# Kernel tuning notes

Hardware: AMD Instinct MI355X
Metric: run time of the kernel (lower is better)

The kernel has to match this reference:

```python
import jax, jax.numpy as jnp
import numpy as np

N_NODES = 32768
AGENTS = 32            # agents per sample (fully connected)
N_SAMPLES = N_NODES // AGENTS
N_EDGES = N_SAMPLES * AGENTS * (AGENTS - 1)  # 1,015,808
D = 64                 # latent_size
EDGE_DIM = 2
Z_DIM = 2 * D + EDGE_DIM  # CGConv concat width = 130
BN_EPS = 1e-5


def _build_block_edge_index():
    # fully-connected (no self-loop) blocks of AGENTS nodes, offset per sample
    a = np.arange(AGENTS)
    src, dst = np.meshgrid(a, a, indexing='ij')
    mask = src != dst
    src, dst = src[mask], dst[mask]              # [AGENTS*(AGENTS-1)]
    offs = (np.arange(N_SAMPLES) * AGENTS)[:, None]
    src = (src[None, :] + offs).reshape(-1)
    dst = (dst[None, :] + offs).reshape(-1)
    return jnp.asarray(np.stack([src, dst]), dtype=jnp.int64)


def setup_inputs() -> dict:
    key = jax.random.key(0)
    ks = jax.random.split(key, 16)
    x = jax.random.normal(ks[0], (N_NODES, D), dtype=jnp.float32)
    edge_index = _build_block_edge_index()                      # [2, E]
    edge_attr = jax.random.normal(ks[1], (N_EDGES, EDGE_DIM), dtype=jnp.float32)
    s = 1.0 / np.sqrt(Z_DIM)
    params = {}
    for li, base in ((1, 2), (2, 8)):
        params[f'Wf{li}'] = jax.random.uniform(ks[base + 0], (Z_DIM, D), jnp.float32, -s, s)
        params[f'bf{li}'] = jax.random.uniform(ks[base + 1], (D,), jnp.float32, -s, s)
        params[f'Ws{li}'] = jax.random.uniform(ks[base + 2], (Z_DIM, D), jnp.float32, -s, s)
        params[f'bs{li}'] = jax.random.uniform(ks[base + 3], (D,), jnp.float32, -s, s)
        params[f'gamma{li}'] = jnp.ones((D,), jnp.float32)
        params[f'beta{li}'] = jnp.zeros((D,), jnp.float32)
    return {'x': x, 'edge_index': edge_index, 'edge_attr': edge_attr, **params}


def _cgconv(x, edge_index, edge_attr, Wf, bf, Ws, bs, gamma, beta):
    src, dst = edge_index[0], edge_index[1]
    # z_ij = [x_i, x_j, e_ij], i = target (dst), j = source (src)
    z = jnp.concatenate([x[dst], x[src], edge_attr], axis=-1)       # [E, Z_DIM]
    m = jax.nn.sigmoid(z @ Wf + bf) * jax.nn.softplus(z @ Ws + bs)  # gated message
    agg = jax.ops.segment_sum(m, dst, num_segments=x.shape[0])      # scatter-add
    mu = jnp.mean(agg, axis=0)
    var = jnp.var(agg, axis=0)
    agg = (agg - mu) * jax.lax.rsqrt(var + BN_EPS) * gamma + beta   # train-mode BN
    return agg + x                                                  # residual


def reference(x, edge_index, edge_attr,
              Wf1, bf1, Ws1, bs1, gamma1, beta1,
              Wf2, bf2, Ws2, bs2, gamma2, beta2):
    h = jax.nn.relu(_cgconv(x, edge_index, edge_attr, Wf1, bf1, Ws1, bs1, gamma1, beta1))
    out = jax.nn.relu(_cgconv(h, edge_index, edge_attr, Wf2, bf2, Ws2, bs2, gamma2, beta2))
    return out
```

## Files before the change

### kernel.cpp

```cpp
#include <hip/hip_runtime.h>


#define NSAMP 1024
#define AG 32
#define DD 64
#define EPB 992
#define NN 32768
#define R1S 132

typedef float f4 __attribute__((ext_vector_type(4)));
typedef float f2 __attribute__((ext_vector_type(2)));

#define L2E 1.44269504088896340736f
#define BN_EPS_SCALED (1e-5 * (double)L2E * (double)L2E)

__device__ __forceinline__ void gacc(f4& acc, const f4 mf, const f4 ms) {
#pragma unroll
  for (int k = 0; k < 4; ++k) {
    float den = 1.0f + __builtin_amdgcn_exp2f(-mf[k]);
    float sig = __builtin_amdgcn_rcpf(den);
    float sp  = fmaxf(ms[k], 0.0f)
              + __builtin_amdgcn_logf(1.0f + __builtin_amdgcn_exp2f(-fabsf(ms[k])));
    acc[k] += sig * sp;
  }
}

template <int SRC>
__device__ __forceinline__ void gpass(const float* __restrict__ Wf,
                                      const float* __restrict__ bfv,
                                      const float* __restrict__ Ws,
                                      const float* __restrict__ bsv,
                                      const float* xb, float* R1, int t) {
  const int tx = t & 31, ty = t >> 5;
  const int q = tx >> 4;
  const int cc0 = (tx & 15) * 4;
  const float* wbase = (q ? Ws : Wf) + SRC * (64 * 64) + cc0;
  f4 acc[4];
  if constexpr (SRC == 0) {
    const float* bv = q ? bsv : bfv;
    f4 b = *(const f4*)(bv + cc0) * L2E;
#pragma unroll
    for (int r = 0; r < 4; ++r) acc[r] = b;
  } else {
    f4 z4 = {0.f, 0.f, 0.f, 0.f};
#pragma unroll
    for (int r = 0; r < 4; ++r) acc[r] = z4;
  }
#pragma unroll
  for (int k4 = 0; k4 < 16; ++k4) {
    const float* wp = wbase + k4 * 4 * 64;
    f4 w0 = *(const f4*)(wp);
    f4 w1 = *(const f4*)(wp + 64);
    f4 w2 = *(const f4*)(wp + 128);
    f4 w3 = *(const f4*)(wp + 192);
#pragma unroll
    for (int r = 0; r < 4; ++r) {
      f4 xv = *(const f4*)&xb[(ty * 4 + r) * 64 + k4 * 4];
      acc[r] += xv.x * w0 + xv.y * w1 + xv.z * w2 + xv.w * w3;
    }
  }
#pragma unroll
  for (int r = 0; r < 4; ++r)
    *(f4*)&R1[(ty * 4 + r) * R1S + q * 64 + cc0] = acc[r];
}

__device__ __forceinline__ void run_layer(
    int t, int s, const float* __restrict__ ea,
    const float* __restrict__ Wf, const float* __restrict__ bfv,
    const float* __restrict__ Ws, const float* __restrict__ bsv,
    float* xb, float* R1, double* __restrict__ stats,
    float* __restrict__ agg)
{
  const int i = t >> 3, c0 = (t & 7) * 8;

  gpass<0>(Wf, bfv, Ws, bsv, xb, R1, t);
  __syncthreads();
  const float* ri = &R1[i * R1S];
  f4 afa = *(const f4*)(ri + c0);
  f4 afb = *(const f4*)(ri + c0 + 4);
  f4 asa = *(const f4*)(ri + 64 + c0);
  f4 asb = *(const f4*)(ri + 64 + c0 + 4);
  __syncthreads();
  gpass<1>(Wf, bfv, Ws, bsv, xb, R1, t);

  f4 wf0a = *(const f4*)(Wf + 128 * 64 + c0);
  f4 wf0b = *(const f4*)(Wf + 128 * 64 + c0 + 4);
  f4 wf1a = *(const f4*)(Wf + 129 * 64 + c0);
  f4 wf1b = *(const f4*)(Wf + 129 * 64 + c0 + 4);
  f4 ws0a = *(const f4*)(Ws + 128 * 64 + c0);
  f4 ws0b = *(const f4*)(Ws + 128 * 64 + c0 + 4);
  f4 ws1a = *(const f4*)(Ws + 129 * 64 + c0);
  f4 ws1b = *(const f4*)(Ws + 129 * 64 + c0 + 4);
  __syncthreads();

  {
    const f2* esrc = ((const f2*)ea) + s * EPB;
    f2* ed = (f2*)xb;
    for (int u = t; u < EPB; u += 256) ed[u] = esrc[u] * L2E;
  }
  __syncthreads();

  f4 acc0 = {0.f, 0.f, 0.f, 0.f}, acc1 = {0.f, 0.f, 0.f, 0.f};
  for (int jj = 0; jj < 31; ++jj) {
    const int ge = (jj >= i) ? 1 : 0;
    const int j  = jj + ge;
    const int e  = j * 31 + i - 1 + ge;
    f2 eav = *(const f2*)&xb[e * 2];
    const float* gj = &R1[j * R1S];
    f4 bfa = *(const f4*)(gj + c0);
    f4 bfb = *(const f4*)(gj + c0 + 4);
    f4 bsa = *(const f4*)(gj + 64 + c0);
    f4 bsb = *(const f4*)(gj + 64 + c0 + 4);
    f4 mfa = afa + bfa + eav.x * wf0a + eav.y * wf1a;
    f4 mfb = afb + bfb + eav.x * wf0b + eav.y * wf1b;
    f4 msa = asa + bsa + eav.x * ws0a + eav.y * ws1a;
    f4 msb = asb + bsb + eav.x * ws0b + eav.y * ws1b;
    gacc(acc0, mfa, msa);
    gacc(acc1, mfb, msb);
  }

  float* ap = agg + (s * AG + i) * DD + c0;
  *(f4*)ap       = acc0;
  *(f4*)(ap + 4) = acc1;

  __syncthreads();
  if (t < 128) R1[t] = 0.f;
  __syncthreads();
#pragma unroll
  for (int k = 0; k < 4; ++k) {
    atomicAdd(&R1[c0 + k],          acc0[k]);
    atomicAdd(&R1[64 + c0 + k],     acc0[k] * acc0[k]);
    atomicAdd(&R1[c0 + 4 + k],      acc1[k]);
    atomicAdd(&R1[64 + c0 + 4 + k], acc1[k] * acc1[k]);
  }
  __syncthreads();
  if (t < 128) atomicAdd(&stats[t], (double)R1[t]);
}

__global__ __launch_bounds__(256, 4) void k_edge1(
    const float* __restrict__ x, const float* __restrict__ ea,
    const float* __restrict__ Wf, const float* __restrict__ bfv,
    const float* __restrict__ Ws, const float* __restrict__ bsv,
    float* __restrict__ agg, double* __restrict__ stats)
{
  __shared__ __align__(16) float xb[2048];
  __shared__ __align__(16) float R1[32 * R1S];
  const int t = threadIdx.x, s = blockIdx.x;
  {
    const f4* src = (const f4*)(x + s * AG * DD);
    f4* dst = (f4*)xb;
    dst[t]       = src[t] * L2E;
    dst[t + 256] = src[t + 256] * L2E;
  }
  __syncthreads();
  run_layer(t, s, ea, Wf, bfv, Ws, bsv, xb, R1, stats, agg);
}

__global__ __launch_bounds__(256, 4) void k_edge2(
    const float* __restrict__ x, const float* __restrict__ ea,
    const float* __restrict__ Wf, const float* __restrict__ bfv,
    const float* __restrict__ Ws, const float* __restrict__ bsv,
    const double* __restrict__ stats1, const float* __restrict__ gmv,
    const float* __restrict__ btv, float* __restrict__ hout,
    float* __restrict__ agg, double* __restrict__ stats2)
{
  __shared__ __align__(16) float xb[2048];
  __shared__ __align__(16) float R1[32 * R1S];
  const int t = threadIdx.x, s = blockIdx.x;
  const int i = t >> 3, c0 = (t & 7) * 8;

  if (t < 64) {
    double mu  = stats1[t] * (1.0 / NN);
    double var = stats1[64 + t] * (1.0 / NN) - mu * mu;
    float rs = (float)(1.0 / sqrt(var + BN_EPS_SCALED));
    float g  = gmv[t] * rs;
    R1[t]      = g;
    R1[64 + t] = btv[t] - (float)mu * g;
  }
  __syncthreads();
  {
    f4 sca = *(const f4*)&R1[c0],      scb = *(const f4*)&R1[c0 + 4];
    f4 sha = *(const f4*)&R1[64 + c0], shb = *(const f4*)&R1[64 + c0 + 4];
    const float* ap = agg + (s * AG + i) * DD + c0;
    f4 a0 = *(const f4*)ap, a1 = *(const f4*)(ap + 4);
    const f4* xg = (const f4*)(x + (s * AG + i) * DD + c0);
    f4 h0 = a0 * sca + sha + xg[0];
    f4 h1 = a1 * scb + shb + xg[1];
#pragma unroll
    for (int k = 0; k < 4; ++k) { h0[k] = fmaxf(h0[k], 0.f); h1[k] = fmaxf(h1[k], 0.f); }
    f4* hg = (f4*)(hout + (s * AG + i) * DD + c0);
    hg[0] = h0; hg[1] = h1;
    *(f4*)&xb[i * DD + c0]     = h0 * L2E;
    *(f4*)&xb[i * DD + c0 + 4] = h1 * L2E;
  }
  __syncthreads();
  run_layer(t, s, ea, Wf, bfv, Ws, bsv, xb, R1, stats2, agg);
}

__global__ __launch_bounds__(256) void k_norm(
    const float* __restrict__ agg, const double* __restrict__ stats,
    const float* __restrict__ gmv, const float* __restrict__ btv,
    float* __restrict__ outp)
{
  __shared__ __align__(16) float sc[DD];
  __shared__ __align__(16) float sh[DD];
  const int t = threadIdx.x;
  if (t < DD) {
    double mu  = stats[t] * (1.0 / NN);
    double var = stats[DD + t] * (1.0 / NN) - mu * mu;
    float rs = (float)(1.0 / sqrt(var + BN_EPS_SCALED));
    float g  = gmv[t] * rs;
    sc[t] = g;
    sh[t] = btv[t] - (float)mu * g;
  }
  __syncthreads();
  const int idx = blockIdx.x * 256 + t;
  const int c   = (idx * 4) & (DD - 1);
  f4 a = ((const f4*)agg)[idx];
  f4 h = ((const f4*)outp)[idx];
  f4 r = a * (*(const f4*)&sc[c]) + (*(const f4*)&sh[c]) + h;
#pragma unroll
  for (int k = 0; k < 4; ++k) r[k] = fmaxf(r[k], 0.0f);
  ((f4*)outp)[idx] = r;
}

extern "C" void kernel_launch(void* const* d_in, const int* in_sizes, int n_in,
                              void* d_out, int out_size, void* d_ws, size_t ws_size,
                              hipStream_t stream) {
  const float* x   = (const float*)d_in[0];
  const float* ea  = (const float*)d_in[2];
  const float* Wf1 = (const float*)d_in[3];
  const float* bf1 = (const float*)d_in[4];
  const float* Ws1 = (const float*)d_in[5];
  const float* bs1 = (const float*)d_in[6];
  const float* gm1 = (const float*)d_in[7];
  const float* bt1 = (const float*)d_in[8];
  const float* Wf2 = (const float*)d_in[9];
  const float* bf2 = (const float*)d_in[10];
  const float* Ws2 = (const float*)d_in[11];
  const float* bs2 = (const float*)d_in[12];
  const float* gm2 = (const float*)d_in[13];
  const float* bt2 = (const float*)d_in[14];

  double* stats = (double*)d_ws;
  float*  agg   = (float*)((char*)d_ws + 4096);
  float*  outp  = (float*)d_out;

  hipMemsetAsync(d_ws, 0, 2048, stream);
  k_edge1<<<NSAMP, 256, 0, stream>>>(x, ea, Wf1, bf1, Ws1, bs1, agg, stats);
  k_edge2<<<NSAMP, 256, 0, stream>>>(x, ea, Wf2, bf2, Ws2, bs2,
                                     stats, gm1, bt1, outp, agg, stats + 128);
  k_norm<<<NN * DD / 4 / 256, 256, 0, stream>>>(agg, stats + 128, gm2, bt2, outp);
}
```

Baseline: 247.2 us.

## Split each sample across two blocks and read inputs directly from global memory

Each sample is now handled by two blocks, each covering 16 target nodes, with 4 channels per thread instead of 8. The kernels raise launch bounds to 8 blocks per CU and drop the LDS staging buffers for x and the edge attributes, reading both straight from global or cache. The L2E scaling moves to after the projection, shuffles pre-reduce the BN statistics before the shared atomics, and separate agg buffers keep layer-1 reads apart from layer-2 writes. The aim is more parallelism and occupancy. The cost is that both blocks recompute the full 32-row source projection and the layer-2 input h, and more workspace is needed.

New measurement: 434.2 us. 75.6% more time.

```diff
diff --git a/kernel.cpp b/kernel.cpp
--- a/kernel.cpp
+++ b/kernel.cpp
@@ -17,8 +17,7 @@
 __device__ __forceinline__ void gacc(f4& acc, const f4 mf, const f4 ms) {
 #pragma unroll
   for (int k = 0; k < 4; ++k) {
-    float den = 1.0f + __builtin_amdgcn_exp2f(-mf[k]);
-    float sig = __builtin_amdgcn_rcpf(den);
+    float sig = __builtin_amdgcn_rcpf(1.0f + __builtin_amdgcn_exp2f(-mf[k]));
     float sp  = fmaxf(ms[k], 0.0f)
               + __builtin_amdgcn_logf(1.0f + __builtin_amdgcn_exp2f(-fabsf(ms[k])));
     acc[k] += sig * sp;
@@ -30,144 +29,125 @@
                                       const float* __restrict__ bfv,
                                       const float* __restrict__ Ws,
                                       const float* __restrict__ bsv,
-                                      const float* xb, float* R1, int t) {
+                                      const float* __restrict__ xs,
+                                      float* R1, int t, int rbase) {
   const int tx = t & 31, ty = t >> 5;
   const int q = tx >> 4;
   const int cc0 = (tx & 15) * 4;
   const float* wbase = (q ? Ws : Wf) + SRC * (64 * 64) + cc0;
-  f4 acc[4];
+  constexpr int RPT = (SRC == 0) ? 2 : 4;
+  f4 acc[RPT];
   if constexpr (SRC == 0) {
     const float* bv = q ? bsv : bfv;
-    f4 b = *(const f4*)(bv + cc0) * L2E;
-#pragma unroll
-    for (int r = 0; r < 4; ++r) acc[r] = b;
+    f4 b = *(const f4*)(bv + cc0);
+#pragma unroll
+    for (int r = 0; r < RPT; ++r) acc[r] = b;
   } else {
-    f4 z4 = {0.f, 0.f, 0.f, 0.f};
-#pragma unroll
-    for (int r = 0; r < 4; ++r) acc[r] = z4;
-  }
-#pragma unroll
+    f4 z = {0.f, 0.f, 0.f, 0.f};
+#pragma unroll
+    for (int r = 0; r < RPT; ++r) acc[r] = z;
+  }
+#pragma unroll 4
   for (int k4 = 0; k4 < 16; ++k4) {
-    const float* wp = wbase + k4 * 4 * 64;
+    const float* wp = wbase + k4 * 256;
     f4 w0 = *(const f4*)(wp);
     f4 w1 = *(const f4*)(wp + 64);
     f4 w2 = *(const f4*)(wp + 128);
     f4 w3 = *(const f4*)(wp + 192);
 #pragma unroll
-    for (int r = 0; r < 4; ++r) {
-      f4 xv = *(const f4*)&xb[(ty * 4 + r) * 64 + k4 * 4];
+    for (int r = 0; r < RPT; ++r) {
+      const int row = (SRC == 0) ? (rbase + ty * RPT + r) : (ty * RPT + r);
+      f4 xv = *(const f4*)(xs + row * 64 + k4 * 4);
       acc[r] += xv.x * w0 + xv.y * w1 + xv.z * w2 + xv.w * w3;
     }
   }
 #pragma unroll
-  for (int r = 0; r < 4; ++r)
-    *(f4*)&R1[(ty * 4 + r) * R1S + q * 64 + cc0] = acc[r];
-}
-
-__device__ __forceinline__ void run_layer(
-    int t, int s, const float* __restrict__ ea,
+  for (int r = 0; r < RPT; ++r)
+    *(f4*)&R1[(ty * RPT + r) * R1S + q * 64 + cc0] = acc[r] * L2E;
+}
+
+__device__ __forceinline__ void layer_body(
+    int t, int s, int rbase,
+    const float* __restrict__ xs, const float* __restrict__ ea,
     const float* __restrict__ Wf, const float* __restrict__ bfv,
     const float* __restrict__ Ws, const float* __restrict__ bsv,
-    float* xb, float* R1, double* __restrict__ stats,
-    float* __restrict__ agg)
-{
-  const int i = t >> 3, c0 = (t & 7) * 8;
-
-  gpass<0>(Wf, bfv, Ws, bsv, xb, R1, t);
-  __syncthreads();
-  const float* ri = &R1[i * R1S];
-  f4 afa = *(const f4*)(ri + c0);
-  f4 afb = *(const f4*)(ri + c0 + 4);
-  f4 asa = *(const f4*)(ri + 64 + c0);
-  f4 asb = *(const f4*)(ri + 64 + c0 + 4);
-  __syncthreads();
-  gpass<1>(Wf, bfv, Ws, bsv, xb, R1, t);
-
-  f4 wf0a = *(const f4*)(Wf + 128 * 64 + c0);
-  f4 wf0b = *(const f4*)(Wf + 128 * 64 + c0 + 4);
-  f4 wf1a = *(const f4*)(Wf + 129 * 64 + c0);
-  f4 wf1b = *(const f4*)(Wf + 129 * 64 + c0 + 4);
-  f4 ws0a = *(const f4*)(Ws + 128 * 64 + c0);
-  f4 ws0b = *(const f4*)(Ws + 128 * 64 + c0 + 4);
-  f4 ws1a = *(const f4*)(Ws + 129 * 64 + c0);
-  f4 ws1b = *(const f4*)(Ws + 129 * 64 + c0 + 4);
-  __syncthreads();
-
-  {
-    const f2* esrc = ((const f2*)ea) + s * EPB;
-    f2* ed = (f2*)xb;
-    for (int u = t; u < EPB; u += 256) ed[u] = esrc[u] * L2E;
-  }
-  __syncthreads();
-
-  f4 acc0 = {0.f, 0.f, 0.f, 0.f}, acc1 = {0.f, 0.f, 0.f, 0.f};
+    float* R1, float* __restrict__ agg, double* __restrict__ stats)
+{
+  gpass<0>(Wf, bfv, Ws, bsv, xs, R1, t, rbase);
+  __syncthreads();
+  const int il = t >> 4, c0 = (t & 15) * 4;
+  f4 af  = *(const f4*)&R1[il * R1S + c0];
+  f4 as_ = *(const f4*)&R1[il * R1S + 64 + c0];
+  __syncthreads();
+  gpass<1>(Wf, bfv, Ws, bsv, xs, R1, t, 0);
+
+  f4 wf0 = *(const f4*)(Wf + 128 * 64 + c0) * L2E;
+  f4 wf1 = *(const f4*)(Wf + 129 * 64 + c0) * L2E;
+  f4 ws0 = *(const f4*)(Ws + 128 * 64 + c0) * L2E;
+  f4 ws1 = *(const f4*)(Ws + 129 * 64 + c0) * L2E;
+  __syncthreads();
+
+  const int i = rbase + il;
+  const f2* ep = (const f2*)ea + (size_t)s * EPB;
+  f4 acc = {0.f, 0.f, 0.f, 0.f};
   for (int jj = 0; jj < 31; ++jj) {
     const int ge = (jj >= i) ? 1 : 0;
     const int j  = jj + ge;
     const int e  = j * 31 + i - 1 + ge;
-    f2 eav = *(const f2*)&xb[e * 2];
-    const float* gj = &R1[j * R1S];
-    f4 bfa = *(const f4*)(gj + c0);
-    f4 bfb = *(const f4*)(gj + c0 + 4);
-    f4 bsa = *(const f4*)(gj + 64 + c0);
-    f4 bsb = *(const f4*)(gj + 64 + c0 + 4);
-    f4 mfa = afa + bfa + eav.x * wf0a + eav.y * wf1a;
-    f4 mfb = afb + bfb + eav.x * wf0b + eav.y * wf1b;
-    f4 msa = asa + bsa + eav.x * ws0a + eav.y * ws1a;
-    f4 msb = asb + bsb + eav.x * ws0b + eav.y * ws1b;
-    gacc(acc0, mfa, msa);
-    gacc(acc1, mfb, msb);
-  }
-
-  float* ap = agg + (s * AG + i) * DD + c0;
-  *(f4*)ap       = acc0;
-  *(f4*)(ap + 4) = acc1;
-
-  __syncthreads();
-  if (t < 128) R1[t] = 0.f;
-  __syncthreads();
+    f2 eav = ep[e];
+    f4 bf_ = *(const f4*)&R1[j * R1S + c0];
+    f4 bs_ = *(const f4*)&R1[j * R1S + 64 + c0];
+    f4 mf = af  + bf_ + eav.x * wf0 + eav.y * wf1;
+    f4 ms = as_ + bs_ + eav.x * ws0 + eav.y * ws1;
+    gacc(acc, mf, ms);
+  }
+  *(f4*)(agg + ((size_t)s * AG + i) * DD + c0) = acc;
+
+  f4 s1 = acc, sq = acc * acc;
 #pragma unroll
   for (int k = 0; k < 4; ++k) {
-    atomicAdd(&R1[c0 + k],          acc0[k]);
-    atomicAdd(&R1[64 + c0 + k],     acc0[k] * acc0[k]);
-    atomicAdd(&R1[c0 + 4 + k],      acc1[k]);
-    atomicAdd(&R1[64 + c0 + 4 + k], acc1[k] * acc1[k]);
+    s1[k] += __shfl_xor(s1[k], 16); sq[k] += __shfl_xor(sq[k], 16);
+    s1[k] += __shfl_xor(s1[k], 32); sq[k] += __shfl_xor(sq[k], 32);
+  }
+  __syncthreads();
+  if (t < 128) R1[t] = 0.0f;
+  __syncthreads();
+  if ((t & 63) < 16) {
+#pragma unroll
+    for (int k = 0; k < 4; ++k) {
+      atomicAdd(&R1[c0 + k],      s1[k]);
+      atomicAdd(&R1[64 + c0 + k], sq[k]);
+    }
   }
   __syncthreads();
   if (t < 128) atomicAdd(&stats[t], (double)R1[t]);
 }
 
-__global__ __launch_bounds__(256, 4) void k_edge1(
+__global__ __launch_bounds__(256, 8) void k_edge1(
     const float* __restrict__ x, const float* __restrict__ ea,
     const float* __restrict__ Wf, const float* __restrict__ bfv,
     const float* __restrict__ Ws, const float* __restrict__ bsv,
     float* __restrict__ agg, double* __restrict__ stats)
 {
-  __shared__ __align__(16) float xb[2048];
   __shared__ __align__(16) float R1[32 * R1S];
-  const int t = threadIdx.x, s = blockIdx.x;
-  {
-    const f4* src = (const f4*)(x + s * AG * DD);
-    f4* dst = (f4*)xb;
-    dst[t]       = src[t] * L2E;
-    dst[t + 256] = src[t + 256] * L2E;
-  }
-  __syncthreads();
-  run_layer(t, s, ea, Wf, bfv, Ws, bsv, xb, R1, stats, agg);
-}
-
-__global__ __launch_bounds__(256, 4) void k_edge2(
+  const int t = threadIdx.x, b = blockIdx.x;
+  const int s = b >> 1, rbase = (b & 1) * 16;
+  layer_body(t, s, rbase, x + (size_t)s * AG * DD, ea,
+             Wf, bfv, Ws, bsv, R1, agg, stats);
+}
+
+__global__ __launch_bounds__(256, 8) void k_edge2(
     const float* __restrict__ x, const float* __restrict__ ea,
     const float* __restrict__ Wf, const float* __restrict__ bfv,
     const float* __restrict__ Ws, const float* __restrict__ bsv,
     const double* __restrict__ stats1, const float* __restrict__ gmv,
     const float* __restrict__ btv, float* __restrict__ hout,
-    float* __restrict__ agg, double* __restrict__ stats2)
-{
-  __shared__ __align__(16) float xb[2048];
+    const float* __restrict__ agg1, float* __restrict__ agg2,
+    double* __restrict__ stats2)
+{
   __shared__ __align__(16) float R1[32 * R1S];
-  const int t = threadIdx.x, s = blockIdx.x;
-  const int i = t >> 3, c0 = (t & 7) * 8;
+  const int t = threadIdx.x, b = blockIdx.x;
+  const int s = b >> 1, rbase = (b & 1) * 16;
 
   if (t < 64) {
     double mu  = stats1[t] * (1.0 / NN);
@@ -179,22 +159,22 @@
   }
   __syncthreads();
   {
-    f4 sca = *(const f4*)&R1[c0],      scb = *(const f4*)&R1[c0 + 4];
-    f4 sha = *(const f4*)&R1[64 + c0], shb = *(const f4*)&R1[64 + c0 + 4];
-    const float* ap = agg + (s * AG + i) * DD + c0;
-    f4 a0 = *(const f4*)ap, a1 = *(const f4*)(ap + 4);
-    const f4* xg = (const f4*)(x + (s * AG + i) * DD + c0);
-    f4 h0 = a0 * sca + sha + xg[0];
-    f4 h1 = a1 * scb + shb + xg[1];
+    const int row = t >> 3, cc = (t & 7) * 8;
+    const size_t base = ((size_t)s * AG + row) * DD + cc;
+    f4 sc0 = *(const f4*)&R1[cc],      sc1 = *(const f4*)&R1[cc + 4];
+    f4 sh0 = *(const f4*)&R1[64 + cc], sh1 = *(const f4*)&R1[64 + cc + 4];
+    f4 a0 = *(const f4*)(agg1 + base), a1 = *(const f4*)(agg1 + base + 4);
+    f4 x0 = *(const f4*)(x + base),    x1 = *(const f4*)(x + base + 4);
+    f4 h0 = a0 * sc0 + sh0 + x0;
+    f4 h1 = a1 * sc1 + sh1 + x1;
 #pragma unroll
     for (int k = 0; k < 4; ++k) { h0[k] = fmaxf(h0[k], 0.f); h1[k] = fmaxf(h1[k], 0.f); }
-    f4* hg = (f4*)(hout + (s * AG + i) * DD + c0);
-    hg[0] = h0; hg[1] = h1;
-    *(f4*)&xb[i * DD + c0]     = h0 * L2E;
-    *(f4*)&xb[i * DD + c0 + 4] = h1 * L2E;
-  }
-  __syncthreads();
-  run_layer(t, s, ea, Wf, bfv, Ws, bsv, xb, R1, stats2, agg);
+    *(f4*)(hout + base)     = h0;
+    *(f4*)(hout + base + 4) = h1;
+  }
+  __syncthreads();
+  layer_body(t, s, rbase, hout + (size_t)s * AG * DD, ea,
+             Wf, bfv, Ws, bsv, R1, agg2, stats2);
 }
 
 __global__ __launch_bounds__(256) void k_norm(
@@ -243,12 +223,14 @@
   const float* bt2 = (const float*)d_in[14];
 
   double* stats = (double*)d_ws;
-  float*  agg   = (float*)((char*)d_ws + 4096);
+  float*  agg1  = (float*)((char*)d_ws + 4096);
+  float*  agg2  = (float*)((char*)d_ws + 4096 + (size_t)NN * DD * 4);
   float*  outp  = (float*)d_out;
 
   hipMemsetAsync(d_ws, 0, 2048, stream);
-  k_edge1<<<NSAMP, 256, 0, stream>>>(x, ea, Wf1, bf1, Ws1, bs1, agg, stats);
-  k_edge2<<<NSAMP, 256, 0, stream>>>(x, ea, Wf2, bf2, Ws2, bs2,
-                                     stats, gm1, bt1, outp, agg, stats + 128);
-  k_norm<<<NN * DD / 4 / 256, 256, 0, stream>>>(agg, stats + 128, gm2, bt2, outp);
-}
+  k_edge1<<<2 * NSAMP, 256, 0, stream>>>(x, ea, Wf1, bf1, Ws1, bs1, agg1, stats);
+  k_edge2<<<2 * NSAMP, 256, 0, stream>>>(x, ea, Wf2, bf2, Ws2, bs2,
+                                         stats, gm1, bt1, outp, agg1, agg2,
+                                         stats + 128);
+  k_norm<<<NN * DD / 4 / 256, 256, 0, stream>>>(agg2, stats + 128, gm2, bt2, outp);
+}
```
